# Performance work log

Hardware: AMD Instinct MI355X
Metric: run time of the kernel (lower is better)

Reference implementation:

```python
import jax, jax.numpy as jnp
import numpy as np

N, C, H, W = 8, 80, 200, 200
PRE_NMS_THRESH = 0.05
PRE_NMS_TOP_N = 1000
NMS_THRESH = 0.6
FPN_POST_NMS_TOP_N = 100
MIN_SIZE = 0.0
TO_REMOVE = 1.0
CLASS_OFFSET = 100000.0  # > any coordinate; separates classes for class-aware NMS


def setup_inputs() -> dict:
    key = jax.random.key(0)
    k1, k2, k3, k4, k5 = jax.random.split(key, 5)
    # logits shifted so sigmoid probs sit near the 0.05 threshold (realistic sparsity)
    box_cls = jax.random.normal(k1, (N, C, H, W), jnp.float32) - 3.0
    box_regression = jax.random.uniform(k2, (N, 4, H, W), jnp.float32) * 64.0
    centerness = jax.random.normal(k3, (N, 1, H, W), jnp.float32)
    locations = jax.random.uniform(k4, (H * W, 2), jnp.float32) * 1600.0
    image_sizes = jax.random.randint(k5, (N, 2), 800, 1600, jnp.int32)  # (h, w)
    return {"locations": locations, "box_cls": box_cls,
            "box_regression": box_regression, "centerness": centerness,
            "image_sizes": image_sizes}


def _pairwise_iou(boxes):
    x1, y1, x2, y2 = boxes[:, 0], boxes[:, 1], boxes[:, 2], boxes[:, 3]
    area = (x2 - x1 + TO_REMOVE) * (y2 - y1 + TO_REMOVE)  # [K]
    iw = jnp.clip(jnp.minimum(x2[:, None], x2[None, :]) - jnp.maximum(x1[:, None], x1[None, :]) + TO_REMOVE, 0.0)
    ih = jnp.clip(jnp.minimum(y2[:, None], y2[None, :]) - jnp.maximum(y1[:, None], y1[None, :]) + TO_REMOVE, 0.0)
    inter = iw * ih
    return inter / (area[:, None] + area[None, :] - inter)


def reference(locations, box_cls, box_regression, centerness, image_sizes):
    n, c, h, w = box_cls.shape
    # [N,C,H,W] -> [N,HW,C] probs; [N,4,H,W] -> [N,HW,4]; centerness -> [N,HW]
    cls_prob = jax.nn.sigmoid(box_cls.transpose(0, 2, 3, 1).reshape(n, -1, c))
    reg = box_regression.transpose(0, 2, 3, 1).reshape(n, -1, 4)
    cent = jax.nn.sigmoid(centerness.transpose(0, 2, 3, 1).reshape(n, -1))

    def per_image(p, r, ct, hw):
        # candidate mask on raw class probs (before centerness weighting), as in source
        cand = p > PRE_NMS_THRESH                      # [HW, C]
        scores = p * ct[:, None]                       # [HW, C]
        flat = jnp.where(cand, scores, -jnp.inf).reshape(-1)
        top_s, top_i = jax.lax.top_k(flat, PRE_NMS_TOP_N)   # sorted desc
        loc_idx = top_i // c
        labels = top_i % c + 1
        valid = top_s > 0.0
        l2 = locations[loc_idx]                        # [K, 2]
        rr = r[loc_idx]                                # [K, 4]
        boxes = jnp.concatenate([l2 - rr[:, :2], l2 + rr[:, 2:]], axis=-1)
        ih = hw[0].astype(jnp.float32)
        iw = hw[1].astype(jnp.float32)
        boxes = jnp.stack([jnp.clip(boxes[:, 0], 0.0, iw - 1.0),
                           jnp.clip(boxes[:, 1], 0.0, ih - 1.0),
                           jnp.clip(boxes[:, 2], 0.0, iw - 1.0),
                           jnp.clip(boxes[:, 3], 0.0, ih - 1.0)], axis=-1)
        bw = boxes[:, 2] - boxes[:, 0] + TO_REMOVE
        bh = boxes[:, 3] - boxes[:, 1] + TO_REMOVE
        valid = valid & (bw >= MIN_SIZE) & (bh >= MIN_SIZE)
        # class-aware NMS via per-class coordinate offset
        ob = boxes + labels.astype(jnp.float32)[:, None] * CLASS_OFFSET
        iou = _pairwise_iou(ob)                        # [K, K]
        K = PRE_NMS_TOP_N
        idxs = jnp.arange(K)
        def body(supp, i):
            keep_i = valid[i] & jnp.logical_not(supp[i])
            supp = supp | (keep_i & (iou[i] > NMS_THRESH) & (idxs != i))
            return supp, keep_i
        _, keep = jax.lax.scan(body, jnp.zeros(K, dtype=bool), idxs)
        fscores = jnp.where(keep & valid, top_s, -jnp.inf)
        fs, fi = jax.lax.top_k(fscores, FPN_POST_NMS_TOP_N)
        fv = fs > 0.0
        fb = boxes[fi] * fv[:, None].astype(boxes.dtype)
        fl = jnp.where(fv, labels[fi], 0).astype(jnp.float32)
        out_s = jnp.where(fv, jnp.sqrt(jnp.where(fv, fs, 1.0)), 0.0)  # sqrt of cls*centerness
        # [K_post, 6] = x1,y1,x2,y2,score,label
        return jnp.concatenate([fb, out_s[:, None], fl[:, None]], axis=-1)

    return jax.vmap(per_image)(cls_prob, reg, cent, image_sizes)
```

## Files before the change

### kernel.cpp

```cpp
#include <hip/hip_runtime.h>
#include <math.h>

#define NIMG 8
#define NCLS 80
#define HW 40000
#define M (NCLS*HW)
#define UBINS 4096
#define CANDL 4096
#define SPILL_CAP 65536
#define BCAP 1024
#define TOPK 1000
#define OUTK 100
#define PRE_T 0.05f
#define NMS_T 0.6f
#define FLOOR_S 0.25f
#define FLOOR_BITS 0x3E800000u
#define FLOOR_SAFE 0.2494f

__device__ unsigned int       g_scnt[NIMG][32];
__device__ unsigned int       g_ovf[NIMG];
__device__ float              g_xthr[NIMG * HW];
__device__ float              g_sct[NIMG * HW];
__device__ unsigned long long g_key[NIMG][SPILL_CAP];

__device__ __forceinline__ float sigmoid_exact(float x){
    return 1.0f / (1.0f + expf(-x));
}

__global__ void k0_init(const float* __restrict__ cent){
    int t = blockIdx.x * blockDim.x + threadIdx.x;
    if (t < NIMG * 32) ((unsigned int*)g_scnt)[t] = 0u;
    if (t < NIMG) g_ovf[t] = 0u;
    if (t < NIMG * HW){
        float pct = sigmoid_exact(cent[t]);
        g_sct[t] = pct;
        float a = FLOOR_SAFE / pct;
        float xt;
        if (a >= 1.0f) xt = 3.0e38f;
        else {
            float am = fminf(a, 0.98f);
            xt = logf(am / (1.0f - am));
        }
        g_xthr[t] = xt;
    }
}

__global__ void __launch_bounds__(1024) k1_spill(const float* __restrict__ cls){
    const int n   = blockIdx.y;
    const int tid = threadIdx.x;
    const int e0  = blockIdx.x * 4096 + tid * 4;
    __shared__ unsigned long long skey[BCAP];
    __shared__ unsigned int lcnt, lbase;
    if (tid == 0) lcnt = 0u;
    __syncthreads();
    if (e0 < M){
        const int c  = e0 / HW;
        const int hw = e0 - c * HW;
        float4 x  = *(const float4*)(cls + (size_t)n * M + e0);
        float4 th = *(const float4*)(g_xthr + n * HW + hw);
        #define SPILL1(J, XV) \
        if (XV >= (J==0?th.x:J==1?th.y:J==2?th.z:th.w)){ \
            float p_ = sigmoid_exact(XV); \
            if (p_ > PRE_T){ \
                float s_ = p_ * g_sct[n * HW + hw + J]; \
                unsigned long long key_ = ((unsigned long long)__float_as_uint(s_) << 32) \
                    | (unsigned long long)(0xFFFFFFFFu - (unsigned int)((hw + J) * NCLS + c)); \
                unsigned int pp_ = atomicAdd(&lcnt, 1u); \
                if (pp_ < BCAP) skey[pp_] = key_; \
            } \
        }
        SPILL1(0, x.x)
        SPILL1(1, x.y)
        SPILL1(2, x.z)
        SPILL1(3, x.w)
        #undef SPILL1
    }
    __syncthreads();
    unsigned int raw = lcnt;
    unsigned int cnt = raw < BCAP ? raw : BCAP;
    if (tid == 0){
        lbase = cnt ? atomicAdd(&g_scnt[n][0], cnt) : 0u;
        if (raw > BCAP) g_ovf[n] = 1u;
    }
    __syncthreads();
    unsigned int base = lbase;
    for (unsigned int i = tid; i < cnt; i += 1024){
        unsigned int pos = base + i;
        if (pos < SPILL_CAP) g_key[n][pos] = skey[i];
    }
}

struct SelPhase {
    unsigned int hist[UBINS];
    unsigned int cs[256];
    unsigned long long keysL[CANDL];
};
struct NmsPhase {
    float ox1[TOPK], oy1[TOPK], ox2[TOPK], oy2[TOPK], oar[TOPK];
    float bxs[TOPK][4];
    float sc[TOPK];
    int   lab[TOPK];
    unsigned char validf[TOPK];
    unsigned char supp[TOPK];
    int   keeplist[OUTK];
};
union KU { SelPhase sel; NmsPhase nms; };

__global__ void __launch_bounds__(1024) k2_select_nms(const float* __restrict__ cls,
                                                      const float* __restrict__ loc,
                                                      const float* __restrict__ reg,
                                                      const int*   __restrict__ imsz,
                                                      float* __restrict__ out){
    const int n = blockIdx.x;
    const int tid = threadIdx.x;
    const int lane = tid & 63;
    __shared__ KU u;
    __shared__ unsigned long long stop[TOPK];
    __shared__ unsigned int lcnt, c025, s_cut, s_flag;

    for (int i = tid; i < UBINS; i += 1024) u.sel.hist[i] = 0u;
    if (tid == 0){ lcnt = 0u; c025 = 0u; }
    if (tid < TOPK) stop[tid] = 0ull;
    __syncthreads();

    unsigned int scnt_raw = g_scnt[n][0];
    unsigned int S = scnt_raw < SPILL_CAP ? scnt_raw : SPILL_CAP;

    for (unsigned int i = tid; i < S; i += 1024){
        unsigned long long k = g_key[n][i];
        unsigned int bits = (unsigned int)(k >> 32);
        float s = __uint_as_float(bits);
        int bin = (int)(s * 4096.0f);
        atomicAdd(&u.sel.hist[bin], 1u);
        unsigned long long mb = __ballot(bits >= FLOOR_BITS);
        if (lane == 0 && mb) atomicAdd(&c025, (unsigned int)__popcll(mb));
    }
    __syncthreads();
    if (tid < 256){
        unsigned int s = 0;
        int base = tid * 16;
        #pragma unroll
        for (int i = 0; i < 16; ++i) s += u.sel.hist[base + i];
        u.sel.cs[tid] = s;
    }
    __syncthreads();
    if (tid == 0){
        unsigned int acc = 0; int cut = 0;
        int c = 255;
        for (; c >= 0; --c){ if (acc + u.sel.cs[c] >= TOPK) break; acc += u.sel.cs[c]; }
        unsigned int Cest = 0;
        if (c >= 0){
            int b = c*16 + 15;
            for (;; --b){
                if (acc + u.sel.hist[b] >= TOPK || b == c*16){ cut = b; break; }
                acc += u.sel.hist[b];
            }
            Cest = acc + u.sel.hist[cut];
        }
        unsigned int fl = (scnt_raw > SPILL_CAP) || g_ovf[n] || (c < 0) ||
                          (c025 < TOPK) || (Cest > CANDL) ? 1u : 0u;
        s_cut = (unsigned int)cut; s_flag = fl;
    }
    __syncthreads();

    if (s_flag){
        for (int i = tid; i < UBINS; i += 1024) u.sel.hist[i] = 0u;
        __syncthreads();
        const float* cls_n = cls + (size_t)n * M;
        const float* sct_n = g_sct + n * HW;
        for (int e = tid; e < M; e += 1024){
            float p = sigmoid_exact(cls_n[e]);
            if (p > PRE_T){
                int c = e / HW; int hw = e - c * HW;
                float s = p * sct_n[hw];
                atomicAdd(&u.sel.hist[(int)(s * 4096.0f)], 1u);
            }
        }
        __syncthreads();
        if (tid < 256){
            unsigned int s = 0;
            int base = tid * 16;
            #pragma unroll
            for (int i = 0; i < 16; ++i) s += u.sel.hist[base + i];
            u.sel.cs[tid] = s;
        }
        __syncthreads();
        if (tid == 0){
            unsigned int acc = 0; int cut = 0; int c = 255;
            for (; c >= 0; --c){ if (acc + u.sel.cs[c] >= TOPK) break; acc += u.sel.cs[c]; }
            if (c >= 0){
                int b = c*16 + 15;
                for (;; --b){ acc += u.sel.hist[b]; if (acc >= TOPK || b == c*16) break; }
                cut = b;
            }
            while (acc > CANDL && cut < UBINS){ acc -= u.sel.hist[cut]; cut++; }
            s_cut = (unsigned int)cut;
        }
        __syncthreads();
        unsigned int cutb = s_cut;
        for (int e = tid; e < M; e += 1024){
            float p = sigmoid_exact(cls_n[e]);
            if (p > PRE_T){
                int c = e / HW; int hw = e - c * HW;
                float s = p * sct_n[hw];
                if ((int)(s * 4096.0f) >= (int)cutb){
                    unsigned int pos = atomicAdd(&lcnt, 1u);
                    if (pos < CANDL){
                        unsigned int idx = (unsigned int)(hw * NCLS + c);
                        u.sel.keysL[pos] = ((unsigned long long)__float_as_uint(s) << 32)
                                         | (unsigned long long)(0xFFFFFFFFu - idx);
                    }
                }
            }
        }
    } else {
        unsigned int cutb = s_cut;
        for (unsigned int i = tid; i < S; i += 1024){
            unsigned long long k = g_key[n][i];
            float s = __uint_as_float((unsigned int)(k >> 32));
            bool pass = ((unsigned int)(int)(s * 4096.0f)) >= cutb;
            unsigned long long mb = __ballot(pass);
            unsigned int wcnt = (unsigned int)__popcll(mb);
            unsigned int base = 0;
            if (lane == 0 && wcnt) base = atomicAdd(&lcnt, wcnt);
            base = (unsigned int)__builtin_amdgcn_readfirstlane((int)base);
            if (pass){
                unsigned int p = base + (unsigned int)__popcll(mb & ((1ull << lane) - 1ull));
                if (p < CANDL) u.sel.keysL[p] = k;
            }
        }
    }
    __syncthreads();

    int C = (int)(lcnt < CANDL ? lcnt : CANDL);
    for (int i = tid; i < C; i += 1024){
        unsigned long long k = u.sel.keysL[i];
        int rank = 0;
        for (int j = 0; j < C; ++j) rank += (u.sel.keysL[j] > k) ? 1 : 0;
        if (rank < TOPK) stop[rank] = k;
    }
    __syncthreads();

    float rx1 = 0.f, ry1 = 0.f, rx2 = -1.f, ry2 = -1.f, rar = 1.f;
    float ihh = (float)imsz[2*n + 0];
    float iww = (float)imsz[2*n + 1];
    unsigned long long kk = (tid < TOPK) ? stop[tid] : 0ull;
    __syncthreads();
    if (tid < TOPK){
        unsigned int bits = (unsigned int)(kk >> 32);
        float s = __uint_as_float(bits);
        u.nms.supp[tid] = 0;
        if (s > 0.0f){
            unsigned int idx = 0xFFFFFFFFu - (unsigned int)(kk & 0xFFFFFFFFull);
            int hw = (int)(idx / NCLS);
            int c  = (int)(idx % NCLS);
            int l  = c + 1;
            float x  = loc[2*hw], y = loc[2*hw + 1];
            float r0 = reg[((size_t)n*4 + 0)*HW + hw];
            float r1 = reg[((size_t)n*4 + 1)*HW + hw];
            float r2 = reg[((size_t)n*4 + 2)*HW + hw];
            float r3 = reg[((size_t)n*4 + 3)*HW + hw];
            float x1 = fminf(fmaxf(x - r0, 0.0f), iww - 1.0f);
            float y1 = fminf(fmaxf(y - r1, 0.0f), ihh - 1.0f);
            float x2 = fminf(fmaxf(x + r2, 0.0f), iww - 1.0f);
            float y2 = fminf(fmaxf(y + r3, 0.0f), ihh - 1.0f);
            u.nms.bxs[tid][0] = x1; u.nms.bxs[tid][1] = y1;
            u.nms.bxs[tid][2] = x2; u.nms.bxs[tid][3] = y2;
            float off = (float)l * 100000.0f;
            float a1 = x1 + off, b1 = y1 + off, a2 = x2 + off, b2 = y2 + off;
            float ar = (a2 - a1 + 1.0f) * (b2 - b1 + 1.0f);
            u.nms.ox1[tid] = a1; u.nms.oy1[tid] = b1;
            u.nms.ox2[tid] = a2; u.nms.oy2[tid] = b2; u.nms.oar[tid] = ar;
            rx1 = a1; ry1 = b1; rx2 = a2; ry2 = b2; rar = ar;
            u.nms.sc[tid] = s; u.nms.lab[tid] = l; u.nms.validf[tid] = 1;
        } else {
            u.nms.validf[tid] = 0; u.nms.sc[tid] = 0.0f; u.nms.lab[tid] = 0;
            u.nms.bxs[tid][0] = u.nms.bxs[tid][1] = 0.0f;
            u.nms.bxs[tid][2] = u.nms.bxs[tid][3] = 0.0f;
            u.nms.ox1[tid] = 0.f; u.nms.oy1[tid] = 0.f;
            u.nms.ox2[tid] = -1.f; u.nms.oy2[tid] = -1.f; u.nms.oar[tid] = 1.f;
        }
    }
    __syncthreads();

    int cnt = 0;
    for (int i = 0; i < TOPK; ++i){
        bool keep_i = u.nms.validf[i] && !u.nms.supp[i];
        if (keep_i){
            if (tid == 0) u.nms.keeplist[cnt] = i;
            if (tid < TOPK && tid != i){
                float ix1 = fmaxf(u.nms.ox1[i], rx1);
                float iy1 = fmaxf(u.nms.oy1[i], ry1);
                float ix2 = fminf(u.nms.ox2[i], rx2);
                float iy2 = fminf(u.nms.oy2[i], ry2);
                float iw_ = fmaxf(ix2 - ix1 + 1.0f, 0.0f);
                float ih_ = fmaxf(iy2 - iy1 + 1.0f, 0.0f);
                float inter = iw_ * ih_;
                float iou = inter / (u.nms.oar[i] + rar - inter);
                if (iou > NMS_T) u.nms.supp[tid] = 1;
            }
            cnt++;
            __syncthreads();
            if (cnt == OUTK) break;
        }
    }
    __syncthreads();

    if (tid < OUTK){
        float r0=0.f,r1=0.f,r2=0.f,r3=0.f,r4=0.f,r5=0.f;
        if (tid < cnt){
            int i = u.nms.keeplist[tid];
            r0 = u.nms.bxs[i][0]; r1 = u.nms.bxs[i][1];
            r2 = u.nms.bxs[i][2]; r3 = u.nms.bxs[i][3];
            r4 = sqrtf(u.nms.sc[i]); r5 = (float)u.nms.lab[i];
        }
        float* o = out + ((size_t)n*OUTK + tid)*6;
        o[0]=r0; o[1]=r1; o[2]=r2; o[3]=r3; o[4]=r4; o[5]=r5;
    }
}

extern "C" void kernel_launch(void* const* d_in, const int* in_sizes, int n_in,
                              void* d_out, int out_size, void* d_ws, size_t ws_size,
                              hipStream_t stream){
    const float* loc  = (const float*)d_in[0];
    const float* cls  = (const float*)d_in[1];
    const float* reg  = (const float*)d_in[2];
    const float* cent = (const float*)d_in[3];
    const int*   imsz = (const int*)d_in[4];
    float* out = (float*)d_out;

    hipLaunchKernelGGL(k0_init,       dim3(625),                 dim3(512),  0, stream, cent);
    hipLaunchKernelGGL(k1_spill,      dim3((M+4095)/4096, NIMG), dim3(1024), 0, stream, cls);
    hipLaunchKernelGGL(k2_select_nms, dim3(NIMG),                dim3(1024), 0, stream,
                       cls, loc, reg, imsz, out);
}
```

Measured before the change: 293.2 us.

## Replace serial NMS with per-class bucketed parallel NMS and persistent spill grid

NMS is restructured: the top-1000 candidates are grouped into per-class buckets (capacity 48), and each of 80 threads runs greedy NMS within its class. Kept boxes are then compacted in score order with a ballot prefix sum. This removes up to 1000 block-wide barrier iterations, and the old serial path remains as a fallback when a bucket overflows. The spill kernel also becomes a grid-stride loop over 256 blocks per image, with a wave-level early-out. This cuts per-block setup and the shared-atomic flush count, but gives up some parallelism.

```diff
diff --git a/kernel.cpp b/kernel.cpp
--- a/kernel.cpp
+++ b/kernel.cpp
@@ -9,13 +9,15 @@
 #define CANDL 4096
 #define SPILL_CAP 65536
 #define BCAP 1024
+#define CCAP 48
 #define TOPK 1000
 #define OUTK 100
 #define PRE_T 0.05f
 #define NMS_T 0.6f
-#define FLOOR_S 0.25f
 #define FLOOR_BITS 0x3E800000u
 #define FLOOR_SAFE 0.2494f
+#define NT1 782
+#define K1GX 256
 
 __device__ unsigned int       g_scnt[NIMG][32];
 __device__ unsigned int       g_ovf[NIMG];
@@ -48,32 +50,42 @@
 __global__ void __launch_bounds__(1024) k1_spill(const float* __restrict__ cls){
     const int n   = blockIdx.y;
     const int tid = threadIdx.x;
-    const int e0  = blockIdx.x * 4096 + tid * 4;
     __shared__ unsigned long long skey[BCAP];
     __shared__ unsigned int lcnt, lbase;
     if (tid == 0) lcnt = 0u;
     __syncthreads();
-    if (e0 < M){
-        const int c  = e0 / HW;
-        const int hw = e0 - c * HW;
-        float4 x  = *(const float4*)(cls + (size_t)n * M + e0);
-        float4 th = *(const float4*)(g_xthr + n * HW + hw);
-        #define SPILL1(J, XV) \
-        if (XV >= (J==0?th.x:J==1?th.y:J==2?th.z:th.w)){ \
-            float p_ = sigmoid_exact(XV); \
-            if (p_ > PRE_T){ \
-                float s_ = p_ * g_sct[n * HW + hw + J]; \
-                unsigned long long key_ = ((unsigned long long)__float_as_uint(s_) << 32) \
-                    | (unsigned long long)(0xFFFFFFFFu - (unsigned int)((hw + J) * NCLS + c)); \
-                unsigned int pp_ = atomicAdd(&lcnt, 1u); \
-                if (pp_ < BCAP) skey[pp_] = key_; \
-            } \
-        }
-        SPILL1(0, x.x)
-        SPILL1(1, x.y)
-        SPILL1(2, x.z)
-        SPILL1(3, x.w)
-        #undef SPILL1
+    const float* cls_n = cls + (size_t)n * M;
+    const float* thr_n = g_xthr + n * HW;
+    const float* sct_n = g_sct  + n * HW;
+    for (int tile = blockIdx.x; tile < NT1; tile += K1GX){
+        int e0 = tile * 4096 + tid * 4;
+        if (e0 < M){
+            int c  = e0 / HW;
+            int hw = e0 - c * HW;
+            float4 x  = *(const float4*)(cls_n + e0);
+            float4 th = *(const float4*)(thr_n + hw);
+            bool s0 = x.x >= th.x, s1 = x.y >= th.y;
+            bool s2 = x.z >= th.z, s3 = x.w >= th.w;
+            if (__any(s0 | s1 | s2 | s3)){
+                float xs[4] = {x.x, x.y, x.z, x.w};
+                bool  ss[4] = {s0, s1, s2, s3};
+                #pragma unroll
+                for (int j = 0; j < 4; ++j){
+                    if (ss[j]){
+                        float p = sigmoid_exact(xs[j]);
+                        if (p > PRE_T){
+                            float s = p * sct_n[hw + j];
+                            unsigned long long key =
+                                ((unsigned long long)__float_as_uint(s) << 32)
+                              | (unsigned long long)(0xFFFFFFFFu -
+                                    (unsigned int)((hw + j) * NCLS + c));
+                            unsigned int pp = atomicAdd(&lcnt, 1u);
+                            if (pp < BCAP) skey[pp] = key;
+                        }
+                    }
+                }
+            }
+        }
     }
     __syncthreads();
     unsigned int raw = lcnt;
@@ -99,10 +111,11 @@
     float ox1[TOPK], oy1[TOPK], ox2[TOPK], oy2[TOPK], oar[TOPK];
     float bxs[TOPK][4];
     float sc[TOPK];
-    int   lab[TOPK];
-    unsigned char validf[TOPK];
-    unsigned char supp[TOPK];
-    int   keeplist[OUTK];
+    unsigned short lab[TOPK];
+    unsigned char  supp[TOPK];
+    unsigned short bucket[NCLS][CCAP];
+    unsigned char  bcnt[NCLS];
+    int keeplist[OUTK];
 };
 union KU { SelPhase sel; NmsPhase nms; };
 
@@ -114,12 +127,14 @@
     const int n = blockIdx.x;
     const int tid = threadIdx.x;
     const int lane = tid & 63;
+    const int wave = tid >> 6;
     __shared__ KU u;
     __shared__ unsigned long long stop[TOPK];
-    __shared__ unsigned int lcnt, c025, s_cut, s_flag;
+    __shared__ unsigned int wsum[16];
+    __shared__ unsigned int lcnt, c025, s_cut, s_flag, s_bovf, s_cnt;
 
     for (int i = tid; i < UBINS; i += 1024) u.sel.hist[i] = 0u;
-    if (tid == 0){ lcnt = 0u; c025 = 0u; }
+    if (tid == 0){ lcnt = 0u; c025 = 0u; s_bovf = 0u; }
     if (tid < TOPK) stop[tid] = 0ull;
     __syncthreads();
 
@@ -130,8 +145,7 @@
         unsigned long long k = g_key[n][i];
         unsigned int bits = (unsigned int)(k >> 32);
         float s = __uint_as_float(bits);
-        int bin = (int)(s * 4096.0f);
-        atomicAdd(&u.sel.hist[bin], 1u);
+        atomicAdd(&u.sel.hist[(int)(s * 4096.0f)], 1u);
         unsigned long long mb = __ballot(bits >= FLOOR_BITS);
         if (lane == 0 && mb) atomicAdd(&c025, (unsigned int)__popcll(mb));
     }
@@ -272,9 +286,9 @@
             u.nms.ox1[tid] = a1; u.nms.oy1[tid] = b1;
             u.nms.ox2[tid] = a2; u.nms.oy2[tid] = b2; u.nms.oar[tid] = ar;
             rx1 = a1; ry1 = b1; rx2 = a2; ry2 = b2; rar = ar;
-            u.nms.sc[tid] = s; u.nms.lab[tid] = l; u.nms.validf[tid] = 1;
+            u.nms.sc[tid] = s; u.nms.lab[tid] = (unsigned short)l;
         } else {
-            u.nms.validf[tid] = 0; u.nms.sc[tid] = 0.0f; u.nms.lab[tid] = 0;
+            u.nms.sc[tid] = 0.0f; u.nms.lab[tid] = 0;
             u.nms.bxs[tid][0] = u.nms.bxs[tid][1] = 0.0f;
             u.nms.bxs[tid][2] = u.nms.bxs[tid][3] = 0.0f;
             u.nms.ox1[tid] = 0.f; u.nms.oy1[tid] = 0.f;
@@ -283,32 +297,85 @@
     }
     __syncthreads();
 
-    int cnt = 0;
-    for (int i = 0; i < TOPK; ++i){
-        bool keep_i = u.nms.validf[i] && !u.nms.supp[i];
-        if (keep_i){
-            if (tid == 0) u.nms.keeplist[cnt] = i;
-            if (tid < TOPK && tid != i){
-                float ix1 = fmaxf(u.nms.ox1[i], rx1);
-                float iy1 = fmaxf(u.nms.oy1[i], ry1);
-                float ix2 = fminf(u.nms.ox2[i], rx2);
-                float iy2 = fminf(u.nms.oy2[i], ry2);
-                float iw_ = fmaxf(ix2 - ix1 + 1.0f, 0.0f);
-                float ih_ = fmaxf(iy2 - iy1 + 1.0f, 0.0f);
-                float inter = iw_ * ih_;
-                float iou = inter / (u.nms.oar[i] + rar - inter);
-                if (iou > NMS_T) u.nms.supp[tid] = 1;
-            }
-            cnt++;
-            __syncthreads();
-            if (cnt == OUTK) break;
-        }
+    if (tid < NCLS){
+        int cnt = 0;
+        for (int i = 0; i < TOPK; ++i){
+            if (u.nms.lab[i] == (unsigned short)(tid + 1) && u.nms.sc[i] > 0.0f){
+                if (cnt < CCAP) u.nms.bucket[tid][cnt] = (unsigned short)i;
+                cnt++;
+            }
+        }
+        u.nms.bcnt[tid] = (unsigned char)(cnt < CCAP ? cnt : CCAP);
+        if (cnt > CCAP) atomicOr(&s_bovf, 1u);
+    }
+    __syncthreads();
+
+    if (!s_bovf){
+        if (tid < NCLS){
+            int kc = u.nms.bcnt[tid];
+            for (int a = 0; a < kc; ++a){
+                int ia = u.nms.bucket[tid][a];
+                if (u.nms.supp[ia]) continue;
+                float ax1 = u.nms.ox1[ia], ay1 = u.nms.oy1[ia];
+                float ax2 = u.nms.ox2[ia], ay2 = u.nms.oy2[ia], aar = u.nms.oar[ia];
+                for (int b = a + 1; b < kc; ++b){
+                    int ib = u.nms.bucket[tid][b];
+                    if (u.nms.supp[ib]) continue;
+                    float ix1 = fmaxf(ax1, u.nms.ox1[ib]);
+                    float iy1 = fmaxf(ay1, u.nms.oy1[ib]);
+                    float ix2 = fminf(ax2, u.nms.ox2[ib]);
+                    float iy2 = fminf(ay2, u.nms.oy2[ib]);
+                    float iw_ = fmaxf(ix2 - ix1 + 1.0f, 0.0f);
+                    float ih_ = fmaxf(iy2 - iy1 + 1.0f, 0.0f);
+                    float inter = iw_ * ih_;
+                    float iou = inter / (aar + u.nms.oar[ib] - inter);
+                    if (iou > NMS_T) u.nms.supp[ib] = 1;
+                }
+            }
+        }
+        __syncthreads();
+        bool kp = (tid < TOPK) && (u.nms.sc[tid] > 0.0f) && !u.nms.supp[tid];
+        unsigned long long mb = __ballot(kp);
+        if (lane == 0) wsum[wave] = (unsigned int)__popcll(mb);
+        __syncthreads();
+        unsigned int pre = 0, tot = 0;
+        for (int w = 0; w < 16; ++w){
+            unsigned int v = wsum[w];
+            if (w < wave) pre += v;
+            tot += v;
+        }
+        pre += (unsigned int)__popcll(mb & ((1ull << lane) - 1ull));
+        if (kp && pre < OUTK) u.nms.keeplist[pre] = tid;
+        if (tid == 0) s_cnt = tot < OUTK ? tot : OUTK;
+    } else {
+        int cnt = 0;
+        for (int i = 0; i < TOPK; ++i){
+            bool keep_i = (u.nms.sc[i] > 0.0f) && !u.nms.supp[i];
+            if (keep_i){
+                if (tid == 0) u.nms.keeplist[cnt] = i;
+                if (tid < TOPK && tid != i){
+                    float ix1 = fmaxf(u.nms.ox1[i], rx1);
+                    float iy1 = fmaxf(u.nms.oy1[i], ry1);
+                    float ix2 = fminf(u.nms.ox2[i], rx2);
+                    float iy2 = fminf(u.nms.oy2[i], ry2);
+                    float iw_ = fmaxf(ix2 - ix1 + 1.0f, 0.0f);
+                    float ih_ = fmaxf(iy2 - iy1 + 1.0f, 0.0f);
+                    float inter = iw_ * ih_;
+                    float iou = inter / (u.nms.oar[i] + rar - inter);
+                    if (iou > NMS_T) u.nms.supp[tid] = 1;
+                }
+                cnt++;
+                __syncthreads();
+                if (cnt == OUTK) break;
+            }
+        }
+        if (tid == 0) s_cnt = cnt;
     }
     __syncthreads();
 
     if (tid < OUTK){
         float r0=0.f,r1=0.f,r2=0.f,r3=0.f,r4=0.f,r5=0.f;
-        if (tid < cnt){
+        if (tid < (int)s_cnt){
             int i = u.nms.keeplist[tid];
             r0 = u.nms.bxs[i][0]; r1 = u.nms.bxs[i][1];
             r2 = u.nms.bxs[i][2]; r3 = u.nms.bxs[i][3];
@@ -329,8 +396,8 @@
     const int*   imsz = (const int*)d_in[4];
     float* out = (float*)d_out;
 
-    hipLaunchKernelGGL(k0_init,       dim3(625),                 dim3(512),  0, stream, cent);
-    hipLaunchKernelGGL(k1_spill,      dim3((M+4095)/4096, NIMG), dim3(1024), 0, stream, cls);
-    hipLaunchKernelGGL(k2_select_nms, dim3(NIMG),                dim3(1024), 0, stream,
+    hipLaunchKernelGGL(k0_init,       dim3(625),        dim3(512),  0, stream, cent);
+    hipLaunchKernelGGL(k1_spill,      dim3(K1GX, NIMG), dim3(1024), 0, stream, cls);
+    hipLaunchKernelGGL(k2_select_nms, dim3(NIMG),       dim3(1024), 0, stream,
                        cls, loc, reg, imsz, out);
 }
```

Result: slower. 396.4 us (+35.2%).
